# Performance work log

Hardware: AMD Instinct MI355X
Metric: run time of the kernel (lower is better)

The kernel has to match this reference:

```python
import jax, jax.numpy as jnp
import numpy as np

N = 50000
E = 800000
D_IN = 128
D_H = 128
D_OUT = 128
G = 64
EPS = 1e-5


def setup_inputs() -> dict:
    key = jax.random.key(0)
    ks = jax.random.split(key, 16)
    s = 0.05
    x = jax.random.normal(ks[0], (N, D_IN), dtype=jnp.float32)
    edge_index = jax.random.randint(ks[1], (2, E), 0, N, dtype=jnp.int64)
    batch = jnp.sort(jax.random.randint(ks[2], (N,), 0, G, dtype=jnp.int64))
    return {
        "x": x,
        "edge_index": edge_index,
        "batch": batch,
        "W1": jax.random.normal(ks[3], (D_IN, D_H), jnp.float32) * s,
        "a_src1": jax.random.normal(ks[4], (D_H,), jnp.float32) * s,
        "a_dst1": jax.random.normal(ks[5], (D_H,), jnp.float32) * s,
        "b1": jnp.zeros((D_H,), jnp.float32),
        "W2": jax.random.normal(ks[6], (D_H, D_H), jnp.float32) * s,
        "a_src2": jax.random.normal(ks[7], (D_H,), jnp.float32) * s,
        "a_dst2": jax.random.normal(ks[8], (D_H,), jnp.float32) * s,
        "b2": jnp.zeros((D_H,), jnp.float32),
        "ln1_g": jnp.ones((D_H,), jnp.float32),
        "ln1_b": jnp.zeros((D_H,), jnp.float32),
        "ln2_g": jnp.ones((D_H,), jnp.float32),
        "ln2_b": jnp.zeros((D_H,), jnp.float32),
        "fc_W": jax.random.normal(ks[9], (D_H, D_OUT), jnp.float32) * s,
        "fc_b": jnp.zeros((D_OUT,), jnp.float32),
        "bn_g": jnp.ones((D_OUT,), jnp.float32),
        "bn_b": jnp.zeros((D_OUT,), jnp.float32),
    }


def gat_conv(x, src, dst, W, a_src, a_dst, b):
    # PyG GATConv, heads=1, concat=False. src=j (message source), dst=i (target).
    h = x @ W                              # [N, C]
    al_s = h @ a_src                       # [N]
    al_d = h @ a_dst                       # [N]
    alpha = jax.nn.leaky_relu(al_s[src] + al_d[dst], 0.2)  # [E']
    m = jax.ops.segment_max(alpha, dst, num_segments=N)    # segment softmax (stable)
    e = jnp.exp(alpha - m[dst])
    z = jax.ops.segment_sum(e, dst, num_segments=N)
    w = e / z[dst]                          # [E']
    out = jax.ops.segment_sum(w[:, None] * h[src], dst, num_segments=N)
    return out + b


def layer_norm(x, g, b):
    mu = jnp.mean(x, axis=-1, keepdims=True)
    var = jnp.mean((x - mu) ** 2, axis=-1, keepdims=True)
    return (x - mu) * jax.lax.rsqrt(var + EPS) * g + b


def reference(x, edge_index, batch, W1, a_src1, a_dst1, b1, W2, a_src2, a_dst2, b2,
              ln1_g, ln1_b, ln2_g, ln2_b, fc_W, fc_b, bn_g, bn_b):
    # add self loops (PyG GATConv default)
    sl = jnp.arange(N, dtype=edge_index.dtype)
    src = jnp.concatenate([edge_index[0], sl])
    dst = jnp.concatenate([edge_index[1], sl])

    h = jax.nn.relu(gat_conv(x, src, dst, W1, a_src1, a_dst1, b1))
    h = layer_norm(h, ln1_g, ln1_b)
    # dropout is identity in eval
    h = gat_conv(h, src, dst, W2, a_src2, a_dst2, b2)
    h = layer_norm(h, ln2_g, ln2_b)
    h = jax.nn.relu(h)

    # global mean pool over graphs
    sums = jax.ops.segment_sum(h, batch, num_segments=G)            # [G, D_H]
    cnts = jax.ops.segment_sum(jnp.ones((N,), h.dtype), batch, num_segments=G)
    pooled = sums / jnp.maximum(cnts, 1.0)[:, None]

    logits = pooled @ fc_W + fc_b                                   # [G, D_OUT]
    # BatchNorm1d (training-mode batch stats, biased variance)
    mu = jnp.mean(logits, axis=0)
    var = jnp.mean((logits - mu) ** 2, axis=0)
    logits = (logits - mu) * jax.lax.rsqrt(var + EPS) * bn_g + bn_b
    return logits
```

## Files before the change

kernel.cpp:

```cpp
#include <hip/hip_runtime.h>
#include <hip/hip_bf16.h>
#include <math.h>

#define N_NODES 50000
#define N_EDGES 800000
#define EN (N_EDGES + N_NODES)
#define D 128
#define G_GRAPHS 64
#define EPS 1e-5f
#define POOL_ROWS_PER_WAVE 64
#define N_TILES 3125

#define NBUCK 196
#define BCAP 8192
#define EPB 4096
#define BIN_BLOCKS ((EN + EPB - 1) / EPB)

typedef short short8 __attribute__((ext_vector_type(8)));
typedef float f32x4  __attribute__((ext_vector_type(4)));
typedef unsigned short us8 __attribute__((ext_vector_type(8)));

__device__ __forceinline__ float wave_reduce_sum(float v) {
  #pragma unroll
  for (int off = 32; off > 0; off >>= 1) v += __shfl_xor(v, off, 64);
  return v;
}
__device__ __forceinline__ float wave_reduce_max(float v) {
  #pragma unroll
  for (int off = 32; off > 0; off >>= 1) v = fmaxf(v, __shfl_xor(v, off, 64));
  return v;
}
__device__ __forceinline__ int wave_reduce_sum_i(int v) {
  #pragma unroll
  for (int off = 32; off > 0; off >>= 1) v += __shfl_xor(v, off, 64);
  return v;
}

__device__ __forceinline__ float bf_to_f(unsigned short u) {
  union { unsigned int i; float f; } a;
  a.i = ((unsigned int)u) << 16;
  return a.f;
}
__device__ __forceinline__ float2 bf2_to_f2(ushort2 u) {
  return make_float2(bf_to_f(u.x), bf_to_f(u.y));
}
__device__ __forceinline__ unsigned short f_to_bf(float f) {
  union { float f; unsigned int i; } v; v.f = f;
  unsigned int r = v.i + 0x7FFF + ((v.i >> 16) & 1);
  return (unsigned short)(r >> 16);
}


__global__ __launch_bounds__(256) void bin_kernel(
    const int* __restrict__ ei, int* __restrict__ gcnt, uint2* __restrict__ bedges) {
  __shared__ int hist[NBUCK], base[NBUCK], curl[NBUCK];
  int tid = threadIdx.x;
  for (int i = tid; i < NBUCK; i += 256) { hist[i] = 0; curl[i] = 0; }
  __syncthreads();
  int e0 = blockIdx.x * EPB;
  int srcs[16], dsts[16];
  #pragma unroll
  for (int i = 0; i < 16; ++i) {
    int e = e0 + i * 256 + tid;
    int s = -1, d = -1;
    if (e < N_EDGES)   { s = ei[e]; d = ei[N_EDGES + e]; }
    else if (e < EN)   { s = e - N_EDGES; d = s; }
    srcs[i] = s; dsts[i] = d;
    if (d >= 0) atomicAdd(&hist[d >> 8], 1);
  }
  __syncthreads();
  for (int i = tid; i < NBUCK; i += 256)
    base[i] = atomicAdd(&gcnt[i], hist[i]);
  __syncthreads();
  #pragma unroll
  for (int i = 0; i < 16; ++i) {
    int d = dsts[i];
    if (d < 0) continue;
    int b = d >> 8;
    int pos = base[b] + atomicAdd(&curl[b], 1);
    if (pos < BCAP) bedges[(size_t)b * BCAP + pos] = make_uint2((unsigned)srcs[i], (unsigned)d);
  }
}

__global__ __launch_bounds__(256) void bucket_csr_kernel(
    const uint2* __restrict__ bedges, const int* __restrict__ gcnt,
    int* __restrict__ offs, int* __restrict__ esrc, float* __restrict__ sums) {
  __shared__ int hist[256], pex[256], curl[256], scanbuf[256];
  __shared__ int wsum[4];
  int b = blockIdx.x, t = threadIdx.x;
  if (b == 0) {
    for (int i = t; i < G_GRAPHS * D; i += 256) sums[i] = 0.f;
    if (t == 0) offs[N_NODES] = EN;
  }
  int pv = (t < b) ? gcnt[t] : 0;
  int v = wave_reduce_sum_i(pv);
  if ((t & 63) == 0) wsum[t >> 6] = v;
  hist[t] = 0; curl[t] = 0;
  __syncthreads();
  int gb = wsum[0] + wsum[1] + wsum[2] + wsum[3];
  int m = gcnt[b]; if (m > BCAP) m = BCAP;
  int node0 = b << 8;
  const uint2* be = bedges + (size_t)b * BCAP;
  for (int k = t; k < m; k += 256) atomicAdd(&hist[be[k].y & 255], 1);
  __syncthreads();
  int h = hist[t];
  scanbuf[t] = h;
  __syncthreads();
  #pragma unroll
  for (int off = 1; off < 256; off <<= 1) {
    int add = (t >= off) ? scanbuf[t - off] : 0;
    __syncthreads();
    scanbuf[t] += add;
    __syncthreads();
  }
  pex[t] = scanbuf[t] - h;
  int node = node0 + t;
  if (node < N_NODES) offs[node] = gb + pex[t];
  __syncthreads();
  for (int k = t; k < m; k += 256) {
    uint2 e = be[k];
    int n = e.y & 255;
    int r = atomicAdd(&curl[n], 1);
    esrc[gb + pex[n] + r] = (int)e.x;
  }
}


__global__ void f2bf_kernel(const float* __restrict__ in, unsigned short* __restrict__ out, int n) {
  int i = blockIdx.x * 256 + threadIdx.x;
  if (i < n) out[i] = f_to_bf(in[i]);
}


__global__ __launch_bounds__(256) void linear_mfma_kernel(
    const unsigned short* __restrict__ Xb, const float* __restrict__ W,
    const float* __restrict__ a_s, const float* __restrict__ a_d,
    unsigned short* __restrict__ Hb, float* __restrict__ AS, float* __restrict__ AD) {
  __shared__ unsigned short Wl[D * D];
  int tid = threadIdx.x;
  #pragma unroll
  for (int it = 0; it < 64; ++it) {
    int flat = it * 256 + tid;
    int r = flat >> 7, col = flat & 127;
    int c = r >> 5, rem = r & 31, quad = rem >> 3, j = rem & 7;
    int t = col >> 4, l = quad * 16 + (col & 15);
    Wl[((t * 4 + c) * 64 + l) * 8 + j] = f_to_bf(W[flat]);
  }
  int lane = tid & 63, wv = tid >> 6;
  int colI = lane & 15, quad = lane >> 4;
  float as_v[8], ad_v[8];
  #pragma unroll
  for (int t = 0; t < 8; ++t) { as_v[t] = a_s[t * 16 + colI]; ad_v[t] = a_d[t * 16 + colI]; }
  __syncthreads();
  for (int tile = blockIdx.x * 4 + wv; tile < N_TILES; tile += gridDim.x * 4) {
    int row0 = tile * 16;
    const unsigned short* xp = Xb + (size_t)(row0 + colI) * D + quad * 8;
    short8 afr[4];
    #pragma unroll
    for (int c = 0; c < 4; ++c) afr[c] = *(const short8*)(xp + c * 32);
    f32x4 acc[8];
    #pragma unroll
    for (int t = 0; t < 8; ++t) acc[t] = (f32x4){0.f, 0.f, 0.f, 0.f};
    #pragma unroll
    for (int t = 0; t < 8; ++t) {
      #pragma unroll
      for (int c = 0; c < 4; ++c) {
        short8 bfr = *(const short8*)&Wl[((t * 4 + c) * 64 + lane) * 8];
        acc[t] = __builtin_amdgcn_mfma_f32_16x16x32_bf16(afr[c], bfr, acc[t], 0, 0, 0);
      }
    }
    #pragma unroll
    for (int r = 0; r < 4; ++r) {
      int row = row0 + quad * 4 + r;
      float s = 0.f, dd = 0.f;
      #pragma unroll
      for (int t = 0; t < 8; ++t) {
        float v = acc[t][r];
        Hb[(size_t)row * D + t * 16 + colI] = f_to_bf(v);
        s  = fmaf(v, as_v[t], s);
        dd = fmaf(v, ad_v[t], dd);
      }
      #pragma unroll
      for (int off = 8; off >= 1; off >>= 1) {
        s  += __shfl_xor(s, off, 64);
        dd += __shfl_xor(dd, off, 64);
      }
      if (colI == 0) { AS[row] = s; AD[row] = dd; }
    }
  }
}


__global__ __launch_bounds__(256) void gat_kernel(
    const unsigned short* __restrict__ Hf, const float* __restrict__ AS,
    const float* __restrict__ AD,
    const int* __restrict__ offs, const int* __restrict__ esrc,
    const float* __restrict__ bias, const float* __restrict__ lng, const float* __restrict__ lnb,
    unsigned short* __restrict__ Out, int relu_after) {
  int tid = threadIdx.x;
  int lane = tid & 63;
  int node = blockIdx.x * 4 + (tid >> 6);
  if (node >= N_NODES) return;
  int beg = offs[node], end = offs[node + 1];
  int deg = end - beg;
  float ald = AD[node];
  int q = lane >> 4, mm = lane & 15;
  float acc[8];
  #pragma unroll
  for (int d = 0; d < 8; ++d) acc[d] = 0.f;
  float z;
  const unsigned short* hq = Hf + 8 * mm;

  if (deg <= 64) {
    int s_l = 0; float a_l = -3.4e38f;
    if (lane < deg) {
      s_l = esrc[beg + lane];
      float a = AS[s_l] + ald;
      a_l = (a > 0.f) ? a : 0.2f * a;
    }
    float mx = wave_reduce_max(a_l);
    float w_l = (lane < deg) ? __expf(a_l - mx) : 0.f;
    z = wave_reduce_sum(w_l);
    int nk4 = (deg + 3) & ~3;
    for (int k = 0; k < nk4; k += 4) {
      int idx = k + q;
      int   s = __shfl(s_l, idx, 64);
      float w = __shfl(w_l, idx, 64);
      us8 hv = *(const us8*)(hq + (size_t)s * D);
      #pragma unroll
      for (int d = 0; d < 8; ++d) acc[d] = fmaf(w, bf_to_f(hv[d]), acc[d]);
    }
  } else {
    float mx = -3.4e38f;
    for (int k = beg + lane; k < end; k += 64) {
      int s = esrc[k];
      float a = AS[s] + ald;
      a = (a > 0.f) ? a : 0.2f * a;
      mx = fmaxf(mx, a);
    }
    mx = wave_reduce_max(mx);
    float zl = 0.f;
    for (int base = beg; base < end; base += 64) {
      int nk = end - base; if (nk > 64) nk = 64;
      int s_l = 0; float w_l = 0.f;
      if (lane < nk) {
        s_l = esrc[base + lane];
        float a = AS[s_l] + ald;
        a = (a > 0.f) ? a : 0.2f * a;
        w_l = __expf(a - mx);
      }
      zl += w_l;
      int nk4 = (nk + 3) & ~3;
      for (int k = 0; k < nk4; k += 4) {
        int idx = k + q;
        int   s = __shfl(s_l, idx, 64);
        float w = __shfl(w_l, idx, 64);
        us8 hv = *(const us8*)(hq + (size_t)s * D);
        #pragma unroll
        for (int d = 0; d < 8; ++d) acc[d] = fmaf(w, bf_to_f(hv[d]), acc[d]);
      }
    }
    z = wave_reduce_sum(zl);
  }

  #pragma unroll
  for (int d = 0; d < 8; ++d) {
    acc[d] += __shfl_xor(acc[d], 16, 64);
    acc[d] += __shfl_xor(acc[d], 32, 64);
  }
  float inv_z = 1.f / z;
  const float4* bp = (const float4*)&bias[8 * mm];
  float4 bA = bp[0], bB = bp[1];
  float bb[8] = {bA.x, bA.y, bA.z, bA.w, bB.x, bB.y, bB.z, bB.w};
  float vv[8];
  #pragma unroll
  for (int d = 0; d < 8; ++d) {
    vv[d] = acc[d] * inv_z + bb[d];
    if (!relu_after) vv[d] = fmaxf(vv[d], 0.f);
  }
  float s8 = 0.f;
  #pragma unroll
  for (int d = 0; d < 8; ++d) s8 += vv[d];
  #pragma unroll
  for (int off = 8; off >= 1; off >>= 1) s8 += __shfl_xor(s8, off, 64);
  float mean = s8 * (1.f / 128.f);
  float v8 = 0.f;
  #pragma unroll
  for (int d = 0; d < 8; ++d) { float dd = vv[d] - mean; v8 += dd * dd; }
  #pragma unroll
  for (int off = 8; off >= 1; off >>= 1) v8 += __shfl_xor(v8, off, 64);
  float inv = rsqrtf(v8 * (1.f / 128.f) + EPS);
  const float4* gp = (const float4*)&lng[8 * mm];
  const float4* lp = (const float4*)&lnb[8 * mm];
  float4 gA = gp[0], gB = gp[1], lA = lp[0], lB = lp[1];
  float gg[8] = {gA.x, gA.y, gA.z, gA.w, gB.x, gB.y, gB.z, gB.w};
  float ll[8] = {lA.x, lA.y, lA.z, lA.w, lB.x, lB.y, lB.z, lB.w};
  us8 o;
  #pragma unroll
  for (int d = 0; d < 8; ++d) {
    float od = (vv[d] - mean) * inv * gg[d] + ll[d];
    if (relu_after) od = fmaxf(od, 0.f);
    o[d] = f_to_bf(od);
  }
  if (q == 0) *(us8*)&Out[(size_t)node * D + 8 * mm] = o;
}


__global__ __launch_bounds__(256) void pool_sum_kernel(
    const unsigned short* __restrict__ Hf, const int* __restrict__ bat,
    float* __restrict__ sums) {
  int lane = threadIdx.x & 63;
  int wv = blockIdx.x * 4 + (threadIdx.x >> 6);
  int r0 = wv * POOL_ROWS_PER_WAVE;
  if (r0 >= N_NODES) return;
  int r1 = r0 + POOL_ROWS_PER_WAVE;
  if (r1 > N_NODES) r1 = N_NODES;
  float acc0 = 0.f, acc1 = 0.f;
  int g = bat[r0];
  for (int r = r0; r < r1; ++r) {
    int gr = bat[r];
    if (gr != g) {
      atomicAdd(&sums[g * D + 2 * lane], acc0);
      atomicAdd(&sums[g * D + 2 * lane + 1], acc1);
      acc0 = 0.f; acc1 = 0.f; g = gr;
    }
    float2 hv = bf2_to_f2(*(const ushort2*)&Hf[(size_t)r * D + 2 * lane]);
    acc0 += hv.x; acc1 += hv.y;
  }
  atomicAdd(&sums[g * D + 2 * lane], acc0);
  atomicAdd(&sums[g * D + 2 * lane + 1], acc1);
}

__device__ __forceinline__ int lower_bound_batch(const int* __restrict__ b, int val) {
  int lo = 0, hi = N_NODES;
  while (lo < hi) {
    int mid = (lo + hi) >> 1;
    if (b[mid] < val) lo = mid + 1; else hi = mid;
  }
  return lo;
}

__global__ void fc_kernel(const float* __restrict__ sums, const int* __restrict__ bat,
                          const float* __restrict__ fcW, const float* __restrict__ fcb,
                          float* __restrict__ logits) {
  int g = blockIdx.x;
  int d = threadIdx.x;
  int start = lower_bound_batch(bat, g);
  int end   = lower_bound_batch(bat, g + 1);
  float cnt = (float)(end - start);
  __shared__ float ps[D];
  ps[d] = sums[g * D + d] / fmaxf(cnt, 1.f);
  __syncthreads();
  float o = fcb[d];
  #pragma unroll 8
  for (int k = 0; k < D; ++k) o = fmaf(ps[k], fcW[k * D + d], o);
  logits[g * D + d] = o;
}

__global__ void bn_kernel(const float* __restrict__ logits, const float* __restrict__ g,
                          const float* __restrict__ b, float* __restrict__ out) {
  int d = threadIdx.x;
  float mu = 0.f;
  for (int i = 0; i < G_GRAPHS; ++i) mu += logits[i * D + d];
  mu *= (1.f / G_GRAPHS);
  float var = 0.f;
  for (int i = 0; i < G_GRAPHS; ++i) { float t = logits[i * D + d] - mu; var += t * t; }
  var *= (1.f / G_GRAPHS);
  float inv = rsqrtf(var + EPS);
  float gg = g[d], bb = b[d];
  for (int i = 0; i < G_GRAPHS; ++i)
    out[i * D + d] = (logits[i * D + d] - mu) * inv * gg + bb;
}


extern "C" void kernel_launch(void* const* d_in, const int* in_sizes, int n_in,
                              void* d_out, int out_size, void* d_ws, size_t ws_size,
                              hipStream_t stream) {
  const float* x    = (const float*)d_in[0];
  const int*   ei   = (const int*)d_in[1];
  const int*   bat  = (const int*)d_in[2];
  const float* W1   = (const float*)d_in[3];
  const float* as1  = (const float*)d_in[4];
  const float* ad1  = (const float*)d_in[5];
  const float* b1   = (const float*)d_in[6];
  const float* W2   = (const float*)d_in[7];
  const float* as2  = (const float*)d_in[8];
  const float* ad2  = (const float*)d_in[9];
  const float* b2   = (const float*)d_in[10];
  const float* ln1g = (const float*)d_in[11];
  const float* ln1b = (const float*)d_in[12];
  const float* ln2g = (const float*)d_in[13];
  const float* ln2b = (const float*)d_in[14];
  const float* fcW  = (const float*)d_in[15];
  const float* fcb  = (const float*)d_in[16];
  const float* bng  = (const float*)d_in[17];
  const float* bnb  = (const float*)d_in[18];

  char* p = (char*)d_ws;
  auto carve = [&](size_t bytes) { char* r = p; p += (bytes + 255) & ~(size_t)255; return r; };
  int*   offs  = (int*)carve((N_NODES + 1) * sizeof(int));
  int*   gcnt  = (int*)carve(NBUCK * sizeof(int));
  int*   esrc  = (int*)carve((size_t)EN * sizeof(int));
  float* AS    = (float*)carve(N_NODES * sizeof(float));
  float* AD    = (float*)carve(N_NODES * sizeof(float));
  float* LG    = (float*)carve((size_t)G_GRAPHS * D * sizeof(float));
  float* SUMS  = (float*)carve((size_t)G_GRAPHS * D * sizeof(float));
  unsigned short* B1b = (unsigned short*)carve((size_t)N_NODES * D * sizeof(unsigned short));
  unsigned short* B2b = (unsigned short*)carve((size_t)N_NODES * D * sizeof(unsigned short));
  uint2* bedges = (uint2*)B1b;

  const int RB = (N_NODES + 3) / 4;
  const int CB = (N_NODES * D + 255) / 256;
  const int PB = (N_NODES + 4 * POOL_ROWS_PER_WAVE - 1) / (4 * POOL_ROWS_PER_WAVE);
  const int LB = 256;

  hipMemsetAsync(gcnt, 0, NBUCK * sizeof(int), stream);
  bin_kernel<<<BIN_BLOCKS, 256, 0, stream>>>(ei, gcnt, bedges);
  bucket_csr_kernel<<<NBUCK, 256, 0, stream>>>(bedges, gcnt, offs, esrc, SUMS);

  f2bf_kernel<<<CB, 256, 0, stream>>>(x, B2b, N_NODES * D);
  linear_mfma_kernel<<<LB, 256, 0, stream>>>(B2b, W1, as1, ad1, B1b, AS, AD);
  gat_kernel<<<RB, 256, 0, stream>>>(B1b, AS, AD, offs, esrc, b1, ln1g, ln1b, B2b, 0);
  linear_mfma_kernel<<<LB, 256, 0, stream>>>(B2b, W2, as2, ad2, B1b, AS, AD);
  gat_kernel<<<RB, 256, 0, stream>>>(B1b, AS, AD, offs, esrc, b2, ln2g, ln2b, B2b, 1);

  pool_sum_kernel<<<PB, 256, 0, stream>>>(B2b, bat, SUMS);
  fc_kernel<<<G_GRAPHS, D, 0, stream>>>(SUMS, bat, fcW, fcb, LG);
  bn_kernel<<<1, D, 0, stream>>>(LG, bng, bnb, (float*)d_out);
}
```

Baseline: 287.4 us.

## Fuse fp32-to-bf16 cast into linear, prefetch gathers, drop max in softmax

Removes the separate f2bf kernel by converting fp32 x to bf16 inside the first linear MFMA kernel's fragment loads. For low-degree nodes the GAT aggregation drops the max-subtraction pass and software-pipelines the neighbour row gathers, two edges per quad-step with next loads issued before the FMAs. LayerNorm computes mean and variance in one fused shuffle reduction using E[x^2]-mean^2. The unstabilised exp and the one-pass variance risk overflow or precision loss if attention logits or activations get large.

```diff
diff --git a/kernel.cpp b/kernel.cpp
--- a/kernel.cpp
+++ b/kernel.cpp
@@ -126,14 +126,9 @@
 }
 
 
-__global__ void f2bf_kernel(const float* __restrict__ in, unsigned short* __restrict__ out, int n) {
-  int i = blockIdx.x * 256 + threadIdx.x;
-  if (i < n) out[i] = f_to_bf(in[i]);
-}
-
-
 __global__ __launch_bounds__(256) void linear_mfma_kernel(
-    const unsigned short* __restrict__ Xb, const float* __restrict__ W,
+    const unsigned short* __restrict__ Xb, const float* __restrict__ Xf,
+    const float* __restrict__ W,
     const float* __restrict__ a_s, const float* __restrict__ a_d,
     unsigned short* __restrict__ Hb, float* __restrict__ AS, float* __restrict__ AD) {
   __shared__ unsigned short Wl[D * D];
@@ -154,10 +149,25 @@
   __syncthreads();
   for (int tile = blockIdx.x * 4 + wv; tile < N_TILES; tile += gridDim.x * 4) {
     int row0 = tile * 16;
-    const unsigned short* xp = Xb + (size_t)(row0 + colI) * D + quad * 8;
     short8 afr[4];
-    #pragma unroll
-    for (int c = 0; c < 4; ++c) afr[c] = *(const short8*)(xp + c * 32);
+    if (Xf) {
+      const float* xpf = Xf + (size_t)(row0 + colI) * D + quad * 8;
+      #pragma unroll
+      for (int c = 0; c < 4; ++c) {
+        float4 f0 = *(const float4*)(xpf + c * 32);
+        float4 f1 = *(const float4*)(xpf + c * 32 + 4);
+        short8 a;
+        a[0] = (short)f_to_bf(f0.x); a[1] = (short)f_to_bf(f0.y);
+        a[2] = (short)f_to_bf(f0.z); a[3] = (short)f_to_bf(f0.w);
+        a[4] = (short)f_to_bf(f1.x); a[5] = (short)f_to_bf(f1.y);
+        a[6] = (short)f_to_bf(f1.z); a[7] = (short)f_to_bf(f1.w);
+        afr[c] = a;
+      }
+    } else {
+      const unsigned short* xp = Xb + (size_t)(row0 + colI) * D + quad * 8;
+      #pragma unroll
+      for (int c = 0; c < 4; ++c) afr[c] = *(const short8*)(xp + c * 32);
+    }
     f32x4 acc[8];
     #pragma unroll
     for (int t = 0; t < 8; ++t) acc[t] = (f32x4){0.f, 0.f, 0.f, 0.f};
@@ -212,24 +222,34 @@
   const unsigned short* hq = Hf + 8 * mm;
 
   if (deg <= 64) {
-    int s_l = 0; float a_l = -3.4e38f;
+    int s_l = 0; float w_l = 0.f;
     if (lane < deg) {
       s_l = esrc[beg + lane];
       float a = AS[s_l] + ald;
-      a_l = (a > 0.f) ? a : 0.2f * a;
-    }
-    float mx = wave_reduce_max(a_l);
-    float w_l = (lane < deg) ? __expf(a_l - mx) : 0.f;
+      a = (a > 0.f) ? a : 0.2f * a;
+      w_l = __expf(a);
+    }
     z = wave_reduce_sum(w_l);
-    int nk4 = (deg + 3) & ~3;
-    for (int k = 0; k < nk4; k += 4) {
-      int idx = k + q;
-      int   s = __shfl(s_l, idx, 64);
-      float w = __shfl(w_l, idx, 64);
-      us8 hv = *(const us8*)(hq + (size_t)s * D);
-      #pragma unroll
-      for (int d = 0; d < 8; ++d) acc[d] = fmaf(w, bf_to_f(hv[d]), acc[d]);
-    }
+    int nsteps = (deg + 7) >> 3;
+    int   sA = __shfl(s_l, q, 64),     sB = __shfl(s_l, 4 + q, 64);
+    float wA = __shfl(w_l, q, 64),     wB = __shfl(w_l, 4 + q, 64);
+    us8 hA = *(const us8*)(hq + (unsigned)sA * D);
+    us8 hB = *(const us8*)(hq + (unsigned)sB * D);
+    for (int k = 1; k < nsteps; ++k) {
+      int   sA1 = __shfl(s_l, 8 * k + q, 64),     sB1 = __shfl(s_l, 8 * k + 4 + q, 64);
+      float wA1 = __shfl(w_l, 8 * k + q, 64),     wB1 = __shfl(w_l, 8 * k + 4 + q, 64);
+      us8 hA1 = *(const us8*)(hq + (unsigned)sA1 * D);
+      us8 hB1 = *(const us8*)(hq + (unsigned)sB1 * D);
+      #pragma unroll
+      for (int d = 0; d < 8; ++d) acc[d] = fmaf(wA, bf_to_f(hA[d]), acc[d]);
+      #pragma unroll
+      for (int d = 0; d < 8; ++d) acc[d] = fmaf(wB, bf_to_f(hB[d]), acc[d]);
+      wA = wA1; wB = wB1; hA = hA1; hB = hB1;
+    }
+    #pragma unroll
+    for (int d = 0; d < 8; ++d) acc[d] = fmaf(wA, bf_to_f(hA[d]), acc[d]);
+    #pragma unroll
+    for (int d = 0; d < 8; ++d) acc[d] = fmaf(wB, bf_to_f(hB[d]), acc[d]);
   } else {
     float mx = -3.4e38f;
     for (int k = beg + lane; k < end; k += 64) {
@@ -255,7 +275,7 @@
         int idx = k + q;
         int   s = __shfl(s_l, idx, 64);
         float w = __shfl(w_l, idx, 64);
-        us8 hv = *(const us8*)(hq + (size_t)s * D);
+        us8 hv = *(const us8*)(hq + (unsigned)s * D);
         #pragma unroll
         for (int d = 0; d < 8; ++d) acc[d] = fmaf(w, bf_to_f(hv[d]), acc[d]);
       }
@@ -270,26 +290,25 @@
   }
   float inv_z = 1.f / z;
   const float4* bp = (const float4*)&bias[8 * mm];
-  float4 bA = bp[0], bB = bp[1];
-  float bb[8] = {bA.x, bA.y, bA.z, bA.w, bB.x, bB.y, bB.z, bB.w};
+  float4 bA4 = bp[0], bB4 = bp[1];
+  float bb[8] = {bA4.x, bA4.y, bA4.z, bA4.w, bB4.x, bB4.y, bB4.z, bB4.w};
   float vv[8];
   #pragma unroll
   for (int d = 0; d < 8; ++d) {
     vv[d] = acc[d] * inv_z + bb[d];
     if (!relu_after) vv[d] = fmaxf(vv[d], 0.f);
   }
-  float s8 = 0.f;
-  #pragma unroll
-  for (int d = 0; d < 8; ++d) s8 += vv[d];
-  #pragma unroll
-  for (int off = 8; off >= 1; off >>= 1) s8 += __shfl_xor(s8, off, 64);
+  float s8 = 0.f, ss = 0.f;
+  #pragma unroll
+  for (int d = 0; d < 8; ++d) { s8 += vv[d]; ss += vv[d] * vv[d]; }
+  #pragma unroll
+  for (int off = 8; off >= 1; off >>= 1) {
+    s8 += __shfl_xor(s8, off, 64);
+    ss += __shfl_xor(ss, off, 64);
+  }
   float mean = s8 * (1.f / 128.f);
-  float v8 = 0.f;
-  #pragma unroll
-  for (int d = 0; d < 8; ++d) { float dd = vv[d] - mean; v8 += dd * dd; }
-  #pragma unroll
-  for (int off = 8; off >= 1; off >>= 1) v8 += __shfl_xor(v8, off, 64);
-  float inv = rsqrtf(v8 * (1.f / 128.f) + EPS);
+  float var = ss * (1.f / 128.f) - mean * mean;
+  float inv = rsqrtf(var + EPS);
   const float4* gp = (const float4*)&lng[8 * mm];
   const float4* lp = (const float4*)&lnb[8 * mm];
   float4 gA = gp[0], gB = gp[1], lA = lp[0], lB = lp[1];
@@ -410,7 +429,6 @@
   uint2* bedges = (uint2*)B1b;
 
   const int RB = (N_NODES + 3) / 4;
-  const int CB = (N_NODES * D + 255) / 256;
   const int PB = (N_NODES + 4 * POOL_ROWS_PER_WAVE - 1) / (4 * POOL_ROWS_PER_WAVE);
   const int LB = 256;
 
@@ -418,10 +436,9 @@
   bin_kernel<<<BIN_BLOCKS, 256, 0, stream>>>(ei, gcnt, bedges);
   bucket_csr_kernel<<<NBUCK, 256, 0, stream>>>(bedges, gcnt, offs, esrc, SUMS);
 
-  f2bf_kernel<<<CB, 256, 0, stream>>>(x, B2b, N_NODES * D);
-  linear_mfma_kernel<<<LB, 256, 0, stream>>>(B2b, W1, as1, ad1, B1b, AS, AD);
+  linear_mfma_kernel<<<LB, 256, 0, stream>>>(nullptr, x, W1, as1, ad1, B1b, AS, AD);
   gat_kernel<<<RB, 256, 0, stream>>>(B1b, AS, AD, offs, esrc, b1, ln1g, ln1b, B2b, 0);
-  linear_mfma_kernel<<<LB, 256, 0, stream>>>(B2b, W2, as2, ad2, B1b, AS, AD);
+  linear_mfma_kernel<<<LB, 256, 0, stream>>>(B2b, nullptr, W2, as2, ad2, B1b, AS, AD);
   gat_kernel<<<RB, 256, 0, stream>>>(B1b, AS, AD, offs, esrc, b2, ln2g, ln2b, B2b, 1);
 
   pool_sum_kernel<<<PB, 256, 0, stream>>>(B2b, bat, SUMS);
```

After: 261.6 us. 9.0% less time.
